# Kernel optimization log

Hardware: AMD Instinct MI355X
Metric: run time of the kernel (lower is better)

The kernel has to match this reference:

```python
import jax, jax.numpy as jnp
import numpy as np

DIM = 3                     # bits consumed per tree level
FBITS = 1 << DIM            # 8 occupancy bits per flag
K = 4                       # set bits per flag (enforced in setup_inputs -> static level sizes)
BITS_PER_DIM = [10, 10, 10]
WORD_LENGTH = sum(BITS_PER_DIM)          # 30
TREE_DEPTH = int(np.ceil(WORD_LENGTH / DIM))  # 10
PERMUTE = np.arange(WORD_LENGTH)[::-1].copy() # bit-reversal permutation
TOTAL_FLAGS = sum(K ** t for t in range(TREE_DEPTH))  # 349525
N_POINTS = K ** TREE_DEPTH                            # 1048576


def _make_flags(total, seed=0):
    # each flag has exactly K of FBITS bits set -> deterministic level sizes
    rng = np.random.default_rng(seed)
    r = rng.random((total, FBITS))
    idx = np.argsort(r, axis=1)[:, :K]          # K distinct bit positions
    flags = np.bitwise_or.reduce(1 << idx, axis=1).astype(np.int32)
    return flags


def setup_inputs() -> dict:
    key = jax.random.key(0)
    k1, k2 = jax.random.split(key)
    flags = jnp.asarray(_make_flags(TOTAL_FLAGS))
    offset = jax.random.normal(k1, (3,), dtype=jnp.float32)
    scale = jax.random.uniform(k2, (3,), dtype=jnp.float32) + 0.5
    return {"flags": flags, "offset": offset, "scale": scale}


def reference(flags, offset, scale):
    bit_range = jnp.arange(FBITS, dtype=jnp.int32)
    X = jnp.zeros((1,), dtype=jnp.int32)
    pos = 0
    # bitops.decode loop: each set bit j of flag i spawns child (X[i] << DIM) | j
    for t in range(TREE_DEPTH):
        n = K ** t  # nodes at this level (static by input construction)
        seg = jax.lax.dynamic_slice(flags, (pos,), (n,))
        bits = (seg[:, None] >> bit_range) & 1            # [n, FBITS]
        i, x = jnp.nonzero(bits == 1, size=n * K)         # row-major, matches tf.where
        X = x.astype(jnp.int32) + (X << DIM)[i]           # [n*K]
        pos += n
    # bitops.permute: scatter each bit b of X to position PERMUTE[b]
    b = (X[:, None] >> jnp.arange(WORD_LENGTH, dtype=jnp.int32)) & 1   # [N, 30]
    X = jnp.sum(b << jnp.asarray(PERMUTE, dtype=jnp.int32), axis=-1)  # [N]
    # bitops.realize: split word into per-dim fields, cast, scale, offset
    masks = jnp.asarray([(1 << bb) - 1 for bb in BITS_PER_DIM], dtype=jnp.int32)
    shifts = jnp.asarray(np.cumsum([0] + BITS_PER_DIM[:-1]), dtype=jnp.int32)
    Xf = ((X[:, None] >> shifts) & masks).astype(jnp.float32)          # [N, 3]
    return Xf * scale + offset
```

## Files before the change

### kernel.cpp

```cpp
#include <hip/hip_runtime.h>


__global__ __launch_bounds__(256) void nbit_tree_decode(
    const int* __restrict__ flags,
    const float* __restrict__ off3,
    const float* __restrict__ scl3,
    float* __restrict__ out)
{
    constexpr unsigned LOFF[9] = {0u, 1u, 5u, 21u, 85u, 341u, 1365u, 5461u, 21845u};

    const unsigned q = blockIdx.x * 256u + threadIdx.x;

    unsigned Xp = 0u;
#pragma unroll
    for (int t = 0; t < 9; ++t) {
        const unsigned i = q >> (18 - 2 * t);
        const unsigned d = (q >> (16 - 2 * t)) & 3u;
        unsigned f = (unsigned)flags[LOFF[t] + i];
        if (d > 0u) f &= f - 1u;
        if (d > 1u) f &= f - 1u;
        if (d > 2u) f &= f - 1u;
        Xp = (Xp << 3) | (unsigned)__builtin_ctz(f);
    }
    unsigned f9 = (unsigned)flags[87381u + q];

    const float s0 = scl3[0], s1 = scl3[1], s2 = scl3[2];
    const float o0 = off3[0], o1 = off3[1], o2 = off3[2];

    float4 v[3];
    float* vf = (float*)v;
    const unsigned base = Xp << 3;
    unsigned f = f9;
#pragma unroll
    for (int d = 0; d < 4; ++d) {
        const unsigned j = (unsigned)__builtin_ctz(f);
        f &= f - 1u;
        const unsigned X  = base | j;
        const unsigned Xr = __brev(X) >> 2;
        vf[3 * d + 0] = fmaf((float)(Xr & 1023u),         s0, o0);
        vf[3 * d + 1] = fmaf((float)((Xr >> 10) & 1023u), s1, o1);
        vf[3 * d + 2] = fmaf((float)((Xr >> 20) & 1023u), s2, o2);
    }

    float4* outv = (float4*)(out + 12u * (size_t)q);
    outv[0] = v[0];
    outv[1] = v[1];
    outv[2] = v[2];
}

extern "C" void kernel_launch(void* const* d_in, const int* in_sizes, int n_in,
                              void* d_out, int out_size, void* d_ws, size_t ws_size,
                              hipStream_t stream) {
    const int*   flags  = (const int*)d_in[0];
    const float* offset = (const float*)d_in[1];
    const float* scale  = (const float*)d_in[2];
    float*       out    = (float*)d_out;

    nbit_tree_decode<<<dim3(1024), dim3(256), 0, stream>>>(flags, offset, scale, out);
}
```

Baseline: 64.70 us.

## Scalarize wave-uniform tree levels and stage output through LDS for coalesced stores

Levels 0 to 5 of the tree walk depend only on bits of the point index that are constant within a wavefront. They now use a readfirstlane copy of the index, so those flag loads and bit selection can run on the scalar unit instead of per lane. The per-thread 48-byte output is written into a swizzled shared-memory buffer, then copied out after a barrier so consecutive threads store consecutive float4s. This is meant to cut redundant vector loads and strided global writes. The cost is an LDS round trip and a block-wide sync.

```diff
diff --git a/kernel.cpp b/kernel.cpp
--- a/kernel.cpp
+++ b/kernel.cpp
@@ -1,5 +1,16 @@
 #include <hip/hip_runtime.h>
 
+
+__device__ __forceinline__ unsigned sel_bit(unsigned f, unsigned d) {
+    if (d > 0u) f &= f - 1u;
+    if (d > 1u) f &= f - 1u;
+    if (d > 2u) f &= f - 1u;
+    return (unsigned)__builtin_ctz(f);
+}
+
+__device__ __forceinline__ unsigned swz(unsigned s) {
+    return s ^ ((s >> 3) & 7u);
+}
 
 __global__ __launch_bounds__(256) void nbit_tree_decode(
     const int* __restrict__ flags,
@@ -7,29 +18,38 @@
     const float* __restrict__ scl3,
     float* __restrict__ out)
 {
-    constexpr unsigned LOFF[9] = {0u, 1u, 5u, 21u, 85u, 341u, 1365u, 5461u, 21845u};
+    constexpr unsigned LOFF[10] = {0u, 1u, 5u, 21u, 85u, 341u, 1365u, 5461u, 21845u, 87381u};
 
-    const unsigned q = blockIdx.x * 256u + threadIdx.x;
+    const unsigned tid = threadIdx.x;
+    const unsigned q = blockIdx.x * 256u + tid;
 
-    unsigned Xp = 0u;
+    const unsigned qw = __builtin_amdgcn_readfirstlane(q);
+    unsigned Xs = 0u;
 #pragma unroll
-    for (int t = 0; t < 9; ++t) {
+    for (int t = 0; t < 6; ++t) {
+        const unsigned i = qw >> (18 - 2 * t);
+        const unsigned d = (qw >> (16 - 2 * t)) & 3u;
+        const unsigned f = (unsigned)flags[LOFF[t] + i];
+        Xs = (Xs << 3) | sel_bit(f, d);
+    }
+
+    unsigned Xv = 0u;
+#pragma unroll
+    for (int t = 6; t < 9; ++t) {
         const unsigned i = q >> (18 - 2 * t);
         const unsigned d = (q >> (16 - 2 * t)) & 3u;
-        unsigned f = (unsigned)flags[LOFF[t] + i];
-        if (d > 0u) f &= f - 1u;
-        if (d > 1u) f &= f - 1u;
-        if (d > 2u) f &= f - 1u;
-        Xp = (Xp << 3) | (unsigned)__builtin_ctz(f);
+        const unsigned f = (unsigned)flags[LOFF[t] + i];
+        Xv = (Xv << 3) | sel_bit(f, d);
     }
-    unsigned f9 = (unsigned)flags[87381u + q];
+    const unsigned base = ((Xs << 9) | Xv) << 3;
+
+    const unsigned f9 = (unsigned)flags[LOFF[9] + q];
 
     const float s0 = scl3[0], s1 = scl3[1], s2 = scl3[2];
     const float o0 = off3[0], o1 = off3[1], o2 = off3[2];
 
     float4 v[3];
     float* vf = (float*)v;
-    const unsigned base = Xp << 3;
     unsigned f = f9;
 #pragma unroll
     for (int d = 0; d < 4; ++d) {
@@ -42,10 +62,18 @@
         vf[3 * d + 2] = fmaf((float)((Xr >> 20) & 1023u), s2, o2);
     }
 
-    float4* outv = (float4*)(out + 12u * (size_t)q);
-    outv[0] = v[0];
-    outv[1] = v[1];
-    outv[2] = v[2];
+    __shared__ float4 stage[768];
+#pragma unroll
+    for (int k = 0; k < 3; ++k)
+        stage[swz(3u * tid + k)] = v[k];
+    __syncthreads();
+
+    float4* og = (float4*)out + (size_t)blockIdx.x * 768u;
+#pragma unroll
+    for (int k = 0; k < 3; ++k) {
+        const unsigned s = 256u * k + tid;
+        og[s] = stage[swz(s)];
+    }
 }
 
 extern "C" void kernel_launch(void* const* d_in, const int* in_sizes, int n_in,
```

Result: no change. 63.72 us (-1.5%).
